# Performance work log

Hardware: AMD Instinct MI355X
Metric: run time of the kernel (lower is better)

## Reference

```python
import jax, jax.numpy as jnp
import numpy as np

N = 100000      # num nodes
R = 32          # num relations
E = 3200000     # num edges
F_IN = 128      # feat_len
H = 16          # hidden dim (hard-coded in source)
C = 8           # num classes


def setup_inputs() -> dict:
    key = jax.random.key(0)
    k1, k2, k3, k4, k5 = jax.random.split(key, 5)
    emb = jax.random.normal(k1, (N, F_IN), dtype=jnp.float32)
    W1 = jax.random.normal(k2, (R, F_IN, H), dtype=jnp.float32) * 0.05
    W2 = jax.random.normal(k3, (R, H, C), dtype=jnp.float32) * 0.05
    edge_index = jax.random.randint(k4, (2, E), 0, N, dtype=jnp.int64)
    edge_type = jax.random.randint(k5, (E,), 0, R, dtype=jnp.int64)
    return {"emb": emb, "W1": W1, "W2": W2,
            "edge_index": edge_index, "edge_type": edge_type}


def _rgcn_layer(x, W, src, dst, etype, edge_norm):
    # x: [N, Fin], W: [R, Fin, Fout]
    # Transform once per relation, then gather per edge (avoids [E,Fin,Fout]).
    xw = jnp.einsum('nf,rfo->rno', x, W)          # [R, N, Fout]
    msg = xw[etype, src] * edge_norm[:, None]      # [E, Fout]
    return jax.ops.segment_sum(msg, dst, num_segments=N)  # [N, Fout]


def reference(emb, W1, W2, edge_index, edge_type):
    src, dst = edge_index[0], edge_index[1]
    # PyG RGCNConv aggr='mean': normalize by per-(dst, relation) in-degree.
    key_idx = dst * R + edge_type                              # [E]
    deg = jax.ops.segment_sum(jnp.ones((E,), emb.dtype), key_idx,
                              num_segments=N * R)              # [N*R]
    edge_norm = 1.0 / jnp.maximum(deg, 1.0)
    edge_norm = edge_norm[key_idx]                             # [E]

    h = jax.nn.relu(_rgcn_layer(emb, W1, src, dst, edge_type, edge_norm))
    h = _rgcn_layer(h, W2, src, dst, edge_type, edge_norm)
    return jax.nn.log_softmax(h, axis=1)
```

## Files before the change

kernel.cpp:

```cpp
#include <hip/hip_runtime.h>
#include <hip/hip_bf16.h>
#include <math.h>

#define N_NODES 100000
#define R 32
#define E_EDGES 3200000
#define F_IN 128
#define HDIM 16
#define CDIM 8
#define NOUT 512
#define M_PAD 100032
#define NBUCK 391
#define CAP 9216
#define KEYS 8192
#define P1CHUNK 8192
#define CVT_BLKS 6252
#define PREP_BLKS 128
#define FRONT_GRID (NBUCK + CVT_BLKS + PREP_BLKS)
#define GEMM_BLKS 1563
#define MID_GRID (NBUCK + GEMM_BLKS)

typedef __attribute__((ext_vector_type(8))) short bf16x8;
typedef __attribute__((ext_vector_type(4))) float f32x4;
typedef __attribute__((ext_vector_type(2))) _Float16 f16x2;

static __device__ __forceinline__ unsigned short f2bf(float f) {
    unsigned int u = __float_as_uint(f);
    unsigned int r = (u + 0x7FFFu + ((u >> 16) & 1u)) >> 16;
    return (unsigned short)r;
}
static __device__ __forceinline__ float bfl(unsigned x) {
    return __uint_as_float(x << 16);
}
static __device__ __forceinline__ float bfh(unsigned x) {
    return __uint_as_float(x & 0xFFFF0000u);
}
static __device__ __forceinline__ f16x2 asf16x2(float f) {
    union { float f; f16x2 h; } u; u.f = f; return u.h;
}

#if __has_builtin(__builtin_amdgcn_fdot2)
static __device__ __forceinline__ float FDOT2(f16x2 a, f16x2 b, float c) {
    return __builtin_amdgcn_fdot2(a, b, c, false);
}
#else
static __device__ __forceinline__ float FDOT2(f16x2 a, f16x2 b, float c) {
    return c + (float)a.x * (float)b.x + (float)a.y * (float)b.y;
}
#endif

__global__ __launch_bounds__(512) void k_front(const int* __restrict__ src,
                                               const int* __restrict__ dst,
                                               const int* __restrict__ et,
                                               const float* __restrict__ emb,
                                               const float* __restrict__ W1,
                                               int* __restrict__ gcursor,
                                               unsigned int* __restrict__ ebuf,
                                               unsigned short* __restrict__ ebf,
                                               unsigned short* __restrict__ BmT) {
    __shared__ int sh[3 * NBUCK];
    int b = blockIdx.x, t = threadIdx.x;
    if (b < NBUCK) {
        int* hist = sh;
        int* rank = sh + NBUCK;
        int* base = sh + 2 * NBUCK;
        for (int j = t; j < NBUCK; j += 512) { hist[j] = 0; rank[j] = 0; }
        __syncthreads();
        int e0 = b * P1CHUNK;
        int e1 = e0 + P1CHUNK; if (e1 > E_EDGES) e1 = E_EDGES;
        int n4 = (e1 - e0) >> 2;
        const int4* d4 = (const int4*)(dst + e0);
        const int4* s4 = (const int4*)(src + e0);
        const int4* t4 = (const int4*)(et + e0);
        for (int i = t; i < n4; i += 512) {
            int4 v = d4[i];
            atomicAdd(&hist[v.x >> 8], 1);
            atomicAdd(&hist[v.y >> 8], 1);
            atomicAdd(&hist[v.z >> 8], 1);
            atomicAdd(&hist[v.w >> 8], 1);
        }
        __syncthreads();
        for (int j = t; j < NBUCK; j += 512)
            base[j] = hist[j] ? atomicAdd(&gcursor[j], hist[j]) : 0;
        __syncthreads();
        for (int i = t; i < n4; i += 512) {
            int4 dv = d4[i];
            int4 sv = s4[i];
            int4 tv = t4[i];
            int ds[4] = {dv.x, dv.y, dv.z, dv.w};
            int ss[4] = {sv.x, sv.y, sv.z, sv.w};
            int ts[4] = {tv.x, tv.y, tv.z, tv.w};
            #pragma unroll
            for (int u = 0; u < 4; ++u) {
                int d = ds[u];
                int bk = d >> 8;
                unsigned pk = ((unsigned)(d & 255) << 22) | ((unsigned)ts[u] << 17)
                            | (unsigned)ss[u];
                int lr = atomicAdd(&rank[bk], 1);
                ebuf[(size_t)bk * CAP + base[bk] + lr] = pk;
            }
        }
    } else if (b < NBUCK + CVT_BLKS) {
        size_t base = ((size_t)(b - NBUCK) * 512 + t) * 4;
        int row = (int)(base >> 7);
        ushort4 o;
        if (row < N_NODES) {
            float4 a = *(const float4*)(emb + base);
            o.x = f2bf(a.x); o.y = f2bf(a.y); o.z = f2bf(a.z); o.w = f2bf(a.w);
        } else {
            o.x = o.y = o.z = o.w = 0;
        }
        *(ushort4*)(ebf + base) = o;
    } else {
        int i = (b - NBUCK - CVT_BLKS) * 512 + t;
        int n = i >> 7;
        int f = i & 127;
        int r = n >> 4;
        int o = n & 15;
        BmT[i] = f2bf(W1[r * (F_IN * HDIM) + f * HDIM + o]);
    }
}

__global__ __launch_bounds__(512) void k_scanb(const int* __restrict__ gcursor,
                                               int* __restrict__ bucketstart,
                                               int* __restrict__ rowstart) {
    __shared__ int sb[NBUCK + 1];
    int t = threadIdx.x;
    if (t == 0) {
        int acc = 0;
        for (int b = 0; b < NBUCK; ++b) { int v = gcursor[b]; sb[b] = acc; acc += v; }
        sb[NBUCK] = acc;
        rowstart[N_NODES] = acc;
    }
    __syncthreads();
    for (int j = t; j <= NBUCK; j += 512) bucketstart[j] = sb[j];
}

__global__ __launch_bounds__(256) void k_mid(const unsigned int* __restrict__ ebuf,
                                             const int* __restrict__ gcursor,
                                             const int* __restrict__ bucketstart,
                                             int* __restrict__ rowstart,
                                             unsigned int* __restrict__ elist,
                                             const unsigned short* __restrict__ Abf,
                                             const unsigned short* __restrict__ BmT,
                                             unsigned short* __restrict__ C) {
    __shared__ __align__(16) char smem[52224 + 64];
    int b = blockIdx.x, t = threadIdx.x;
    if (b < NBUCK) {
        unsigned int* cnt = (unsigned int*)smem;
        int* wsum = (int*)(smem + 32768);
        int cntE = gcursor[b];
        size_t esrc = (size_t)b * CAP;
        int e0 = bucketstart[b];
        #pragma unroll
        for (int j = 0; j < KEYS / 256; ++j) cnt[t + j * 256] = 0;
        __syncthreads();
        for (int i = t; i < cntE; i += 256)
            atomicAdd(&cnt[ebuf[esrc + i] >> 17], 1u);
        __syncthreads();
        int kbase = t * (KEYS / 256);
        int s = 0;
        #pragma unroll
        for (int j = 0; j < KEYS / 256; ++j) s += (int)cnt[kbase + j];
        int lane = t & 63, wv = t >> 6;
        int sc = s;
        #pragma unroll
        for (int off = 1; off < 64; off <<= 1) {
            int v = __shfl_up(sc, off, 64);
            if (lane >= off) sc += v;
        }
        if (lane == 63) wsum[wv] = sc;
        __syncthreads();
        if (t == 0) {
            int a = 0;
            #pragma unroll
            for (int w = 0; w < 4; ++w) { int v = wsum[w]; wsum[w] = a; a += v; }
        }
        __syncthreads();
        int run = wsum[wv] + sc - s;
        #pragma unroll
        for (int j = 0; j < KEYS / 256; ++j) {
            unsigned v = cnt[kbase + j];
            unsigned lc = v > 1023u ? 1023u : v;
            cnt[kbase + j] = (unsigned)run | (lc << 20);
            run += (int)v;
        }
        __syncthreads();
        {
            int d = b * 256 + t;
            if (d < N_NODES) rowstart[d] = e0 + (int)(cnt[t * 32] & 0xFFFFFu);
        }
        __syncthreads();
        for (int i = t; i < cntE; i += 256) {
            unsigned pk = ebuf[esrc + i];
            int key = pk >> 17;
            unsigned vv = atomicAdd(&cnt[key], 1u);
            int pos = (int)(vv & 0xFFFFFu);
            unsigned len = (vv >> 20) & 1023u;
            elist[e0 + pos] = (pk & 0x3FFFFFu) | (len << 22);
        }
    } else {
        unsigned short* As = (unsigned short*)smem;
        unsigned short* Bs = (unsigned short*)(smem + 17408);
        int row0 = (b - NBUCK) * 64;
        #pragma unroll
        for (int j = 0; j < 4; ++j) {
            int idx = t + j * 256;
            int r = idx >> 4;
            int u = idx & 15;
            float4 v = *(const float4*)(Abf + (size_t)(row0 + r) * F_IN + u * 8);
            *(float4*)(&As[r * 136 + u * 8]) = v;
        }
        int w = t >> 6;
        int lane = t & 63;
        int q = lane >> 4;
        int mr = lane & 15;
        const unsigned short* ap = &As[(w * 16 + mr) * 136 + q * 8];
        for (int col0 = 0; col0 < NOUT; col0 += 128) {
            __syncthreads();
            #pragma unroll
            for (int j = 0; j < 8; ++j) {
                int idx = t + j * 256;
                int r = idx >> 4;
                int u = idx & 15;
                float4 v = *(const float4*)(BmT + (size_t)(col0 + r) * F_IN + u * 8);
                *(float4*)(&Bs[r * 136 + u * 8]) = v;
            }
            __syncthreads();
            f32x4 acc[8] = {};
            #pragma unroll
            for (int kk = 0; kk < 4; ++kk) {
                bf16x8 af = *(const bf16x8*)(ap + kk * 32);
                #pragma unroll
                for (int tt = 0; tt < 8; ++tt) {
                    bf16x8 bf = *(const bf16x8*)(&Bs[(tt * 16 + mr) * 136 + q * 8 + kk * 32]);
                    acc[tt] = __builtin_amdgcn_mfma_f32_16x16x32_bf16(af, bf, acc[tt], 0, 0, 0);
                }
            }
            #pragma unroll
            for (int tt = 0; tt < 8; ++tt) {
                #pragma unroll
                for (int j = 0; j < 4; ++j) {
                    int row = row0 + w * 16 + q * 4 + j;
                    C[(size_t)row * NOUT + col0 + tt * 16 + mr] = f2bf(acc[tt][j]);
                }
            }
        }
    }
}

__global__ __launch_bounds__(256) void k_gather1(const int* __restrict__ rowstart,
                                                 const unsigned int* __restrict__ elist,
                                                 const unsigned short* __restrict__ xw1,
                                                 _Float16* __restrict__ h) {
    __shared__ float nlut[1024];
    int t = threadIdx.x;
    for (int j = t; j < 1024; j += 256) nlut[j] = 1.0f / (float)(j ? j : 1);
    __syncthreads();
    int g = t >> 3;
    int c = t & 7;
    int d = blockIdx.x * 32 + g;
    if (d >= N_NODES) return;
    int i = rowstart[d], end = rowstart[d + 1];
    float a0 = 0.f, a1 = 0.f, b0 = 0.f, b1 = 0.f;
    float c0 = 0.f, c1 = 0.f, e0 = 0.f, e1 = 0.f;
    for (; i + 3 < end; i += 4) {
        unsigned pk0 = elist[i];
        unsigned pk1 = elist[i + 1];
        unsigned pk2 = elist[i + 2];
        unsigned pk3 = elist[i + 3];
        unsigned x0 = *(const unsigned*)(xw1 + (size_t)(pk0 & 0x1FFFF) * NOUT + ((pk0 >> 17) & 31) * HDIM + c * 2);
        unsigned x1 = *(const unsigned*)(xw1 + (size_t)(pk1 & 0x1FFFF) * NOUT + ((pk1 >> 17) & 31) * HDIM + c * 2);
        unsigned x2 = *(const unsigned*)(xw1 + (size_t)(pk2 & 0x1FFFF) * NOUT + ((pk2 >> 17) & 31) * HDIM + c * 2);
        unsigned x3 = *(const unsigned*)(xw1 + (size_t)(pk3 & 0x1FFFF) * NOUT + ((pk3 >> 17) & 31) * HDIM + c * 2);
        float n0 = nlut[pk0 >> 22], n1 = nlut[pk1 >> 22];
        float n2 = nlut[pk2 >> 22], n3 = nlut[pk3 >> 22];
        a0 += bfl(x0) * n0; a1 += bfh(x0) * n0;
        b0 += bfl(x1) * n1; b1 += bfh(x1) * n1;
        c0 += bfl(x2) * n2; c1 += bfh(x2) * n2;
        e0 += bfl(x3) * n3; e1 += bfh(x3) * n3;
    }
    for (; i < end; ++i) {
        unsigned pk = elist[i];
        unsigned x = *(const unsigned*)(xw1 + (size_t)(pk & 0x1FFFF) * NOUT + ((pk >> 17) & 31) * HDIM + c * 2);
        float nm = nlut[pk >> 22];
        a0 += bfl(x) * nm; a1 += bfh(x) * nm;
    }
    f16x2 o;
    o.x = (_Float16)fmaxf(a0 + b0 + c0 + e0, 0.f);
    o.y = (_Float16)fmaxf(a1 + b1 + c1 + e1, 0.f);
    *(f16x2*)(h + (size_t)d * HDIM + c * 2) = o;
}

#define W2P 260
__global__ __launch_bounds__(256) void k_gather2(const int* __restrict__ rowstart,
                                                 const unsigned int* __restrict__ elist,
                                                 const _Float16* __restrict__ h,
                                                 const float* __restrict__ W2,
                                                 float* __restrict__ out) {
    __shared__ f16x2 sW2h[CDIM * W2P];
    __shared__ float nlut[1024];
    int t = threadIdx.x;
    for (int j = t; j < 1024; j += 256) nlut[j] = 1.0f / (float)(j ? j : 1);
    #pragma unroll
    for (int j = 0; j < 8; ++j) {
        int idx = t + j * 256;
        int c = idx >> 8;
        int rem = idx & 255;
        int r = rem >> 3;
        int jj = rem & 7;
        f16x2 p;
        p.x = (_Float16)W2[r * (HDIM * CDIM) + (2 * jj) * CDIM + c];
        p.y = (_Float16)W2[r * (HDIM * CDIM) + (2 * jj + 1) * CDIM + c];
        sW2h[c * W2P + rem] = p;
    }
    __syncthreads();

    int g = t >> 3;
    int c = t & 7;
    int d = blockIdx.x * 32 + g;
    if (d >= N_NODES) return;
    const f16x2* wc = &sW2h[c * W2P];
    int i = rowstart[d], end = rowstart[d + 1];
    float acc0 = 0.f, acc1 = 0.f, acc2 = 0.f, acc3 = 0.f;
    for (; i + 3 < end; i += 4) {
        unsigned pk0 = elist[i];
        unsigned pk1 = elist[i + 1];
        unsigned pk2 = elist[i + 2];
        unsigned pk3 = elist[i + 3];
        const float4* hp0 = (const float4*)(h + (size_t)(pk0 & 0x1FFFF) * HDIM);
        const float4* hp1 = (const float4*)(h + (size_t)(pk1 & 0x1FFFF) * HDIM);
        const float4* hp2 = (const float4*)(h + (size_t)(pk2 & 0x1FFFF) * HDIM);
        const float4* hp3 = (const float4*)(h + (size_t)(pk3 & 0x1FFFF) * HDIM);
        float4 u0 = hp0[0], u1 = hp0[1];
        float4 v0 = hp1[0], v1 = hp1[1];
        float4 w0 = hp2[0], w1 = hp2[1];
        float4 x0 = hp3[0], x1 = hp3[1];
        float nm0 = nlut[pk0 >> 22], nm1 = nlut[pk1 >> 22];
        float nm2 = nlut[pk2 >> 22], nm3 = nlut[pk3 >> 22];
        const f16x2* wp0 = wc + ((pk0 >> 17) & 31) * 8;
        const f16x2* wp1 = wc + ((pk1 >> 17) & 31) * 8;
        const f16x2* wp2 = wc + ((pk2 >> 17) & 31) * 8;
        const f16x2* wp3 = wc + ((pk3 >> 17) & 31) * 8;
        float s0 = 0.f, s1 = 0.f, s2 = 0.f, s3 = 0.f;
        s0 = FDOT2(asf16x2(u0.x), wp0[0], s0);
        s0 = FDOT2(asf16x2(u0.y), wp0[1], s0);
        s0 = FDOT2(asf16x2(u0.z), wp0[2], s0);
        s0 = FDOT2(asf16x2(u0.w), wp0[3], s0);
        s0 = FDOT2(asf16x2(u1.x), wp0[4], s0);
        s0 = FDOT2(asf16x2(u1.y), wp0[5], s0);
        s0 = FDOT2(asf16x2(u1.z), wp0[6], s0);
        s0 = FDOT2(asf16x2(u1.w), wp0[7], s0);
        s1 = FDOT2(asf16x2(v0.x), wp1[0], s1);
        s1 = FDOT2(asf16x2(v0.y), wp1[1], s1);
        s1 = FDOT2(asf16x2(v0.z), wp1[2], s1);
        s1 = FDOT2(asf16x2(v0.w), wp1[3], s1);
        s1 = FDOT2(asf16x2(v1.x), wp1[4], s1);
        s1 = FDOT2(asf16x2(v1.y), wp1[5], s1);
        s1 = FDOT2(asf16x2(v1.z), wp1[6], s1);
        s1 = FDOT2(asf16x2(v1.w), wp1[7], s1);
        s2 = FDOT2(asf16x2(w0.x), wp2[0], s2);
        s2 = FDOT2(asf16x2(w0.y), wp2[1], s2);
        s2 = FDOT2(asf16x2(w0.z), wp2[2], s2);
        s2 = FDOT2(asf16x2(w0.w), wp2[3], s2);
        s2 = FDOT2(asf16x2(w1.x), wp2[4], s2);
        s2 = FDOT2(asf16x2(w1.y), wp2[5], s2);
        s2 = FDOT2(asf16x2(w1.z), wp2[6], s2);
        s2 = FDOT2(asf16x2(w1.w), wp2[7], s2);
        s3 = FDOT2(asf16x2(x0.x), wp3[0], s3);
        s3 = FDOT2(asf16x2(x0.y), wp3[1], s3);
        s3 = FDOT2(asf16x2(x0.z), wp3[2], s3);
        s3 = FDOT2(asf16x2(x0.w), wp3[3], s3);
        s3 = FDOT2(asf16x2(x1.x), wp3[4], s3);
        s3 = FDOT2(asf16x2(x1.y), wp3[5], s3);
        s3 = FDOT2(asf16x2(x1.z), wp3[6], s3);
        s3 = FDOT2(asf16x2(x1.w), wp3[7], s3);
        acc0 += nm0 * s0;
        acc1 += nm1 * s1;
        acc2 += nm2 * s2;
        acc3 += nm3 * s3;
    }
    for (; i < end; ++i) {
        unsigned pk = elist[i];
        const float4* hp = (const float4*)(h + (size_t)(pk & 0x1FFFF) * HDIM);
        float4 u0 = hp[0], u1 = hp[1];
        float nm = nlut[pk >> 22];
        const f16x2* wp = wc + ((pk >> 17) & 31) * 8;
        float sd = 0.f;
        sd = FDOT2(asf16x2(u0.x), wp[0], sd);
        sd = FDOT2(asf16x2(u0.y), wp[1], sd);
        sd = FDOT2(asf16x2(u0.z), wp[2], sd);
        sd = FDOT2(asf16x2(u0.w), wp[3], sd);
        sd = FDOT2(asf16x2(u1.x), wp[4], sd);
        sd = FDOT2(asf16x2(u1.y), wp[5], sd);
        sd = FDOT2(asf16x2(u1.z), wp[6], sd);
        sd = FDOT2(asf16x2(u1.w), wp[7], sd);
        acc0 += nm * sd;
    }
    float acc = (acc0 + acc1) + (acc2 + acc3);
    float m = acc;
    #pragma unroll
    for (int mask = 1; mask < 8; mask <<= 1)
        m = fmaxf(m, __shfl_xor(m, mask, 8));
    float ex = expf(acc - m);
    float ssumv = ex;
    #pragma unroll
    for (int mask = 1; mask < 8; mask <<= 1)
        ssumv += __shfl_xor(ssumv, mask, 8);
    out[(size_t)d * CDIM + c] = acc - m - logf(ssumv);
}

extern "C" void kernel_launch(void* const* d_in, const int* in_sizes, int n_in,
                              void* d_out, int out_size, void* d_ws, size_t ws_size,
                              hipStream_t stream) {
    const float* emb = (const float*)d_in[0];
    const float* W1  = (const float*)d_in[1];
    const float* W2  = (const float*)d_in[2];
    const int* ei    = (const int*)d_in[3];
    const int* et    = (const int*)d_in[4];
    const int* srcp  = ei;
    const int* dstp  = ei + E_EDGES;

    char* ws = (char*)d_ws;
    size_t off = 0;
    #define ALIGN256(x) (((x) + 255) & ~(size_t)255)
    int* gcursor     = (int*)(ws + off); off = ALIGN256(off + 512 * 4);
    int* bucketstart = (int*)(ws + off); off = ALIGN256(off + 512 * 4);
    int* rowstart    = (int*)(ws + off); off = ALIGN256(off + ((size_t)N_NODES + 8) * 4);
    unsigned int* ebuf  = (unsigned int*)(ws + off); off = ALIGN256(off + (size_t)NBUCK * CAP * 4);
    unsigned int* elist = (unsigned int*)(ws + off); off = ALIGN256(off + (size_t)E_EDGES * 4);
    unsigned short* BmT  = (unsigned short*)(ws + off); off = ALIGN256(off + (size_t)NOUT * F_IN * 2);
    unsigned short* ebf  = (unsigned short*)(ws + off); off = ALIGN256(off + (size_t)M_PAD * F_IN * 2);
    unsigned short* xw1  = (unsigned short*)(ws + off); off = ALIGN256(off + (size_t)M_PAD * NOUT * 2);
    _Float16* h          = (_Float16*)(ws + off);       off = ALIGN256(off + (size_t)N_NODES * HDIM * 2);
    float* out = (float*)d_out;

    hipMemsetAsync(gcursor, 0, 512 * 4, stream);

    k_front<<<FRONT_GRID, 512, 0, stream>>>(srcp, dstp, et, emb, W1, gcursor, ebuf, ebf, BmT);
    k_scanb<<<1, 512, 0, stream>>>(gcursor, bucketstart, rowstart);
    k_mid<<<MID_GRID, 256, 0, stream>>>(ebuf, gcursor, bucketstart, rowstart, elist, ebf, BmT, xw1);
    k_gather1<<<(N_NODES + 31) / 32, 256, 0, stream>>>(rowstart, elist, xw1, h);
    k_gather2<<<(N_NODES + 31) / 32, 256, 0, stream>>>(rowstart, elist, h, W2, out);
}
```

Before: 328.3 us.

## Fuse emb conversion into GEMM, drop scan kernel, group layer-2 gather by relation

Removes the separate fp32-to-bf16 conversion of emb by converting inside the k_mid GEMM tile load, and drops the k_scanb kernel by keeping a per-bucket fixed-capacity edge list with per-node (start,end) pairs. Layer-2 gather now sums h rows per (dst,relation) run in fp16 before applying W2 once per run, using a transposed W2 table in shared memory. This saves memory passes, one launch and per-edge dot products, but accumulates in fp16 and makes the run loop serial per node, which reduces memory-level parallelism.

```diff
diff --git a/kernel.cpp b/kernel.cpp
--- a/kernel.cpp
+++ b/kernel.cpp
@@ -14,9 +14,8 @@
 #define CAP 9216
 #define KEYS 8192
 #define P1CHUNK 8192
-#define CVT_BLKS 6252
 #define PREP_BLKS 128
-#define FRONT_GRID (NBUCK + CVT_BLKS + PREP_BLKS)
+#define FRONT_GRID (NBUCK + PREP_BLKS)
 #define GEMM_BLKS 1563
 #define MID_GRID (NBUCK + GEMM_BLKS)
 
@@ -38,6 +37,9 @@
 static __device__ __forceinline__ f16x2 asf16x2(float f) {
     union { float f; f16x2 h; } u; u.f = f; return u.h;
 }
+static __device__ __forceinline__ float asflt(f16x2 h) {
+    union { f16x2 h; float f; } u; u.h = h; return u.f;
+}
 
 #if __has_builtin(__builtin_amdgcn_fdot2)
 static __device__ __forceinline__ float FDOT2(f16x2 a, f16x2 b, float c) {
@@ -52,11 +54,9 @@
 __global__ __launch_bounds__(512) void k_front(const int* __restrict__ src,
                                                const int* __restrict__ dst,
                                                const int* __restrict__ et,
-                                               const float* __restrict__ emb,
                                                const float* __restrict__ W1,
                                                int* __restrict__ gcursor,
                                                unsigned int* __restrict__ ebuf,
-                                               unsigned short* __restrict__ ebf,
                                                unsigned short* __restrict__ BmT) {
     __shared__ int sh[3 * NBUCK];
     int b = blockIdx.x, t = threadIdx.x;
@@ -100,19 +100,8 @@
                 ebuf[(size_t)bk * CAP + base[bk] + lr] = pk;
             }
         }
-    } else if (b < NBUCK + CVT_BLKS) {
-        size_t base = ((size_t)(b - NBUCK) * 512 + t) * 4;
-        int row = (int)(base >> 7);
-        ushort4 o;
-        if (row < N_NODES) {
-            float4 a = *(const float4*)(emb + base);
-            o.x = f2bf(a.x); o.y = f2bf(a.y); o.z = f2bf(a.z); o.w = f2bf(a.w);
-        } else {
-            o.x = o.y = o.z = o.w = 0;
-        }
-        *(ushort4*)(ebf + base) = o;
     } else {
-        int i = (b - NBUCK - CVT_BLKS) * 512 + t;
+        int i = (b - NBUCK) * 512 + t;
         int n = i >> 7;
         int f = i & 127;
         int r = n >> 4;
@@ -121,27 +110,11 @@
     }
 }
 
-__global__ __launch_bounds__(512) void k_scanb(const int* __restrict__ gcursor,
-                                               int* __restrict__ bucketstart,
-                                               int* __restrict__ rowstart) {
-    __shared__ int sb[NBUCK + 1];
-    int t = threadIdx.x;
-    if (t == 0) {
-        int acc = 0;
-        for (int b = 0; b < NBUCK; ++b) { int v = gcursor[b]; sb[b] = acc; acc += v; }
-        sb[NBUCK] = acc;
-        rowstart[N_NODES] = acc;
-    }
-    __syncthreads();
-    for (int j = t; j <= NBUCK; j += 512) bucketstart[j] = sb[j];
-}
-
 __global__ __launch_bounds__(256) void k_mid(const unsigned int* __restrict__ ebuf,
                                              const int* __restrict__ gcursor,
-                                             const int* __restrict__ bucketstart,
-                                             int* __restrict__ rowstart,
+                                             int2* __restrict__ rse,
                                              unsigned int* __restrict__ elist,
-                                             const unsigned short* __restrict__ Abf,
+                                             const float* __restrict__ A,
                                              const unsigned short* __restrict__ BmT,
                                              unsigned short* __restrict__ C) {
     __shared__ __align__(16) char smem[52224 + 64];
@@ -150,13 +123,12 @@
         unsigned int* cnt = (unsigned int*)smem;
         int* wsum = (int*)(smem + 32768);
         int cntE = gcursor[b];
-        size_t esrc = (size_t)b * CAP;
-        int e0 = bucketstart[b];
+        size_t e0 = (size_t)b * CAP;
         #pragma unroll
         for (int j = 0; j < KEYS / 256; ++j) cnt[t + j * 256] = 0;
         __syncthreads();
         for (int i = t; i < cntE; i += 256)
-            atomicAdd(&cnt[ebuf[esrc + i] >> 17], 1u);
+            atomicAdd(&cnt[ebuf[e0 + i] >> 17], 1u);
         __syncthreads();
         int kbase = t * (KEYS / 256);
         int s = 0;
@@ -188,11 +160,15 @@
         __syncthreads();
         {
             int d = b * 256 + t;
-            if (d < N_NODES) rowstart[d] = e0 + (int)(cnt[t * 32] & 0xFFFFFu);
+            if (d < N_NODES) {
+                int rs = (int)(cnt[t * 32] & 0xFFFFFu);
+                int re = (t < 255) ? (int)(cnt[(t + 1) * 32] & 0xFFFFFu) : cntE;
+                rse[d] = make_int2((int)e0 + rs, (int)e0 + re);
+            }
         }
         __syncthreads();
         for (int i = t; i < cntE; i += 256) {
-            unsigned pk = ebuf[esrc + i];
+            unsigned pk = ebuf[e0 + i];
             int key = pk >> 17;
             unsigned vv = atomicAdd(&cnt[key], 1u);
             int pos = (int)(vv & 0xFFFFFu);
@@ -204,12 +180,16 @@
         unsigned short* Bs = (unsigned short*)(smem + 17408);
         int row0 = (b - NBUCK) * 64;
         #pragma unroll
-        for (int j = 0; j < 4; ++j) {
+        for (int j = 0; j < 8; ++j) {
             int idx = t + j * 256;
-            int r = idx >> 4;
-            int u = idx & 15;
-            float4 v = *(const float4*)(Abf + (size_t)(row0 + r) * F_IN + u * 8);
-            *(float4*)(&As[r * 136 + u * 8]) = v;
+            int r = idx >> 5;
+            int u = idx & 31;
+            int grow = row0 + r;
+            float4 v = make_float4(0.f, 0.f, 0.f, 0.f);
+            if (grow < N_NODES) v = *(const float4*)(A + (size_t)grow * F_IN + u * 4);
+            ushort4 o;
+            o.x = f2bf(v.x); o.y = f2bf(v.y); o.z = f2bf(v.z); o.w = f2bf(v.w);
+            *(ushort4*)(&As[r * 136 + u * 4]) = o;
         }
         int w = t >> 6;
         int lane = t & 63;
@@ -249,7 +229,7 @@
     }
 }
 
-__global__ __launch_bounds__(256) void k_gather1(const int* __restrict__ rowstart,
+__global__ __launch_bounds__(256) void k_gather1(const int2* __restrict__ rse,
                                                  const unsigned int* __restrict__ elist,
                                                  const unsigned short* __restrict__ xw1,
                                                  _Float16* __restrict__ h) {
@@ -261,7 +241,8 @@
     int c = t & 7;
     int d = blockIdx.x * 32 + g;
     if (d >= N_NODES) return;
-    int i = rowstart[d], end = rowstart[d + 1];
+    int2 rr = rse[d];
+    int i = rr.x, end = rr.y;
     float a0 = 0.f, a1 = 0.f, b0 = 0.f, b1 = 0.f;
     float c0 = 0.f, c1 = 0.f, e0 = 0.f, e1 = 0.f;
     for (; i + 3 < end; i += 4) {
@@ -292,27 +273,25 @@
     *(f16x2*)(h + (size_t)d * HDIM + c * 2) = o;
 }
 
-#define W2P 260
-__global__ __launch_bounds__(256) void k_gather2(const int* __restrict__ rowstart,
+__global__ __launch_bounds__(256) void k_gather2(const int2* __restrict__ rse,
                                                  const unsigned int* __restrict__ elist,
                                                  const _Float16* __restrict__ h,
                                                  const float* __restrict__ W2,
                                                  float* __restrict__ out) {
-    __shared__ f16x2 sW2h[CDIM * W2P];
+    __shared__ f16x2 w2t[64 * 33];
     __shared__ float nlut[1024];
     int t = threadIdx.x;
     for (int j = t; j < 1024; j += 256) nlut[j] = 1.0f / (float)(j ? j : 1);
     #pragma unroll
     for (int j = 0; j < 8; ++j) {
         int idx = t + j * 256;
-        int c = idx >> 8;
-        int rem = idx & 255;
-        int r = rem >> 3;
-        int jj = rem & 7;
+        int k = idx >> 8;
+        int c = (idx >> 5) & 7;
+        int r = idx & 31;
         f16x2 p;
-        p.x = (_Float16)W2[r * (HDIM * CDIM) + (2 * jj) * CDIM + c];
-        p.y = (_Float16)W2[r * (HDIM * CDIM) + (2 * jj + 1) * CDIM + c];
-        sW2h[c * W2P + rem] = p;
+        p.x = (_Float16)W2[r * 128 + (2 * k) * 8 + c];
+        p.y = (_Float16)W2[r * 128 + (2 * k + 1) * 8 + c];
+        w2t[(k * 8 + c) * 33 + r] = p;
     }
     __syncthreads();
 
@@ -320,84 +299,29 @@
     int c = t & 7;
     int d = blockIdx.x * 32 + g;
     if (d >= N_NODES) return;
-    const f16x2* wc = &sW2h[c * W2P];
-    int i = rowstart[d], end = rowstart[d + 1];
-    float acc0 = 0.f, acc1 = 0.f, acc2 = 0.f, acc3 = 0.f;
-    for (; i + 3 < end; i += 4) {
-        unsigned pk0 = elist[i];
-        unsigned pk1 = elist[i + 1];
-        unsigned pk2 = elist[i + 2];
-        unsigned pk3 = elist[i + 3];
-        const float4* hp0 = (const float4*)(h + (size_t)(pk0 & 0x1FFFF) * HDIM);
-        const float4* hp1 = (const float4*)(h + (size_t)(pk1 & 0x1FFFF) * HDIM);
-        const float4* hp2 = (const float4*)(h + (size_t)(pk2 & 0x1FFFF) * HDIM);
-        const float4* hp3 = (const float4*)(h + (size_t)(pk3 & 0x1FFFF) * HDIM);
-        float4 u0 = hp0[0], u1 = hp0[1];
-        float4 v0 = hp1[0], v1 = hp1[1];
-        float4 w0 = hp2[0], w1 = hp2[1];
-        float4 x0 = hp3[0], x1 = hp3[1];
-        float nm0 = nlut[pk0 >> 22], nm1 = nlut[pk1 >> 22];
-        float nm2 = nlut[pk2 >> 22], nm3 = nlut[pk3 >> 22];
-        const f16x2* wp0 = wc + ((pk0 >> 17) & 31) * 8;
-        const f16x2* wp1 = wc + ((pk1 >> 17) & 31) * 8;
-        const f16x2* wp2 = wc + ((pk2 >> 17) & 31) * 8;
-        const f16x2* wp3 = wc + ((pk3 >> 17) & 31) * 8;
-        float s0 = 0.f, s1 = 0.f, s2 = 0.f, s3 = 0.f;
-        s0 = FDOT2(asf16x2(u0.x), wp0[0], s0);
-        s0 = FDOT2(asf16x2(u0.y), wp0[1], s0);
-        s0 = FDOT2(asf16x2(u0.z), wp0[2], s0);
-        s0 = FDOT2(asf16x2(u0.w), wp0[3], s0);
-        s0 = FDOT2(asf16x2(u1.x), wp0[4], s0);
-        s0 = FDOT2(asf16x2(u1.y), wp0[5], s0);
-        s0 = FDOT2(asf16x2(u1.z), wp0[6], s0);
-        s0 = FDOT2(asf16x2(u1.w), wp0[7], s0);
-        s1 = FDOT2(asf16x2(v0.x), wp1[0], s1);
-        s1 = FDOT2(asf16x2(v0.y), wp1[1], s1);
-        s1 = FDOT2(asf16x2(v0.z), wp1[2], s1);
-        s1 = FDOT2(asf16x2(v0.w), wp1[3], s1);
-        s1 = FDOT2(asf16x2(v1.x), wp1[4], s1);
-        s1 = FDOT2(asf16x2(v1.y), wp1[5], s1);
-        s1 = FDOT2(asf16x2(v1.z), wp1[6], s1);
-        s1 = FDOT2(asf16x2(v1.w), wp1[7], s1);
-        s2 = FDOT2(asf16x2(w0.x), wp2[0], s2);
-        s2 = FDOT2(asf16x2(w0.y), wp2[1], s2);
-        s2 = FDOT2(asf16x2(w0.z), wp2[2], s2);
-        s2 = FDOT2(asf16x2(w0.w), wp2[3], s2);
-        s2 = FDOT2(asf16x2(w1.x), wp2[4], s2);
-        s2 = FDOT2(asf16x2(w1.y), wp2[5], s2);
-        s2 = FDOT2(asf16x2(w1.z), wp2[6], s2);
-        s2 = FDOT2(asf16x2(w1.w), wp2[7], s2);
-        s3 = FDOT2(asf16x2(x0.x), wp3[0], s3);
-        s3 = FDOT2(asf16x2(x0.y), wp3[1], s3);
-        s3 = FDOT2(asf16x2(x0.z), wp3[2], s3);
-        s3 = FDOT2(asf16x2(x0.w), wp3[3], s3);
-        s3 = FDOT2(asf16x2(x1.x), wp3[4], s3);
-        s3 = FDOT2(asf16x2(x1.y), wp3[5], s3);
-        s3 = FDOT2(asf16x2(x1.z), wp3[6], s3);
-        s3 = FDOT2(asf16x2(x1.w), wp3[7], s3);
-        acc0 += nm0 * s0;
-        acc1 += nm1 * s1;
-        acc2 += nm2 * s2;
-        acc3 += nm3 * s3;
-    }
-    for (; i < end; ++i) {
+    int2 rr = rse[d];
+    int i = rr.x, end = rr.y;
+    float acc = 0.f;
+    while (i < end) {
         unsigned pk = elist[i];
-        const float4* hp = (const float4*)(h + (size_t)(pk & 0x1FFFF) * HDIM);
-        float4 u0 = hp[0], u1 = hp[1];
-        float nm = nlut[pk >> 22];
-        const f16x2* wp = wc + ((pk >> 17) & 31) * 8;
-        float sd = 0.f;
-        sd = FDOT2(asf16x2(u0.x), wp[0], sd);
-        sd = FDOT2(asf16x2(u0.y), wp[1], sd);
-        sd = FDOT2(asf16x2(u0.z), wp[2], sd);
-        sd = FDOT2(asf16x2(u0.w), wp[3], sd);
-        sd = FDOT2(asf16x2(u1.x), wp[4], sd);
-        sd = FDOT2(asf16x2(u1.y), wp[5], sd);
-        sd = FDOT2(asf16x2(u1.z), wp[6], sd);
-        sd = FDOT2(asf16x2(u1.w), wp[7], sd);
-        acc0 += nm * sd;
-    }
-    float acc = (acc0 + acc1) + (acc2 + acc3);
+        int r = (pk >> 17) & 31;
+        int len = pk >> 22;
+        float nm = nlut[len];
+        int stop = i + len;
+        f16x2 hs = {(_Float16)0.f, (_Float16)0.f};
+        for (; i < stop; ++i) {
+            int s = elist[i] & 0x1FFFF;
+            hs += *(const f16x2*)(h + (size_t)s * HDIM + c * 2);
+        }
+        float hvf = asflt(hs);
+        float runsum = 0.f;
+        #pragma unroll
+        for (int k = 0; k < 8; ++k) {
+            float hvk = __shfl(hvf, k, 8);
+            runsum = FDOT2(asf16x2(hvk), w2t[(k * 8 + c) * 33 + r], runsum);
+        }
+        acc += nm * runsum;
+    }
     float m = acc;
     #pragma unroll
     for (int mask = 1; mask < 8; mask <<= 1)
@@ -425,21 +349,18 @@
     size_t off = 0;
     #define ALIGN256(x) (((x) + 255) & ~(size_t)255)
     int* gcursor     = (int*)(ws + off); off = ALIGN256(off + 512 * 4);
-    int* bucketstart = (int*)(ws + off); off = ALIGN256(off + 512 * 4);
-    int* rowstart    = (int*)(ws + off); off = ALIGN256(off + ((size_t)N_NODES + 8) * 4);
+    int2* rse        = (int2*)(ws + off); off = ALIGN256(off + ((size_t)N_NODES + 8) * 8);
     unsigned int* ebuf  = (unsigned int*)(ws + off); off = ALIGN256(off + (size_t)NBUCK * CAP * 4);
-    unsigned int* elist = (unsigned int*)(ws + off); off = ALIGN256(off + (size_t)E_EDGES * 4);
+    unsigned int* elist = (unsigned int*)(ws + off); off = ALIGN256(off + (size_t)NBUCK * CAP * 4);
     unsigned short* BmT  = (unsigned short*)(ws + off); off = ALIGN256(off + (size_t)NOUT * F_IN * 2);
-    unsigned short* ebf  = (unsigned short*)(ws + off); off = ALIGN256(off + (size_t)M_PAD * F_IN * 2);
     unsigned short* xw1  = (unsigned short*)(ws + off); off = ALIGN256(off + (size_t)M_PAD * NOUT * 2);
     _Float16* h          = (_Float16*)(ws + off);       off = ALIGN256(off + (size_t)N_NODES * HDIM * 2);
     float* out = (float*)d_out;
 
     hipMemsetAsync(gcursor, 0, 512 * 4, stream);
 
-    k_front<<<FRONT_GRID, 512, 0, stream>>>(srcp, dstp, et, emb, W1, gcursor, ebuf, ebf, BmT);
-    k_scanb<<<1, 512, 0, stream>>>(gcursor, bucketstart, rowstart);
-    k_mid<<<MID_GRID, 256, 0, stream>>>(ebuf, gcursor, bucketstart, rowstart, elist, ebf, BmT, xw1);
-    k_gather1<<<(N_NODES + 31) / 32, 256, 0, stream>>>(rowstart, elist, xw1, h);
-    k_gather2<<<(N_NODES + 31) / 32, 256, 0, stream>>>(rowstart, elist, h, W2, out);
-}
+    k_front<<<FRONT_GRID, 512, 0, stream>>>(srcp, dstp, et, W1, gcursor, ebuf, BmT);
+    k_mid<<<MID_GRID, 256, 0, stream>>>(ebuf, gcursor, rse, elist, emb, BmT, xw1);
+    k_gather1<<<(N_NODES + 31) / 32, 256, 0, stream>>>(rse, elist, xw1, h);
+    k_gather2<<<(N_NODES + 31) / 32, 256, 0, stream>>>(rse, elist, h, W2, out);
+}
```

New measurement: 391.5 us. +19.2%, slower.
